# Optimization experiments

Hardware: AMD Instinct MI355X
Metric: run time of the kernel (lower is better)

The kernel has to match this reference:

```python
import jax, jax.numpy as jnp
import numpy as np

S = 2          # scale_int = ceil(scale)
K = 3          # kernel size
OUTC = 3       # num_out_ch
NUM_FEAT = 64


def conv3x3(x, w, b):
    y = jax.lax.conv_general_dilated(x, w, (1, 1), ((1, 1), (1, 1)),
                                     dimension_numbers=('NCHW', 'OIHW', 'NCHW'))
    return y + b[None, :, None, None]


def unfold3x3(x):
    # torch F.unfold(x, 3, padding=1): (N, C*9, H*W), order c*9 + ki*3 + kj
    N, C, H, W = x.shape
    xp = jnp.pad(x, ((0, 0), (0, 0), (1, 1), (1, 1)))
    patches = jnp.stack([xp[:, :, i:i + H, j:j + W]
                         for i in range(3) for j in range(3)], axis=2)  # (N,C,9,H,W)
    return patches.reshape(N, C * 9, H * W)


def setup_inputs() -> dict:
    key = jax.random.key(0)
    ks = jax.random.split(key, 12)
    b, t, c, h, w = 2, 4, 16, 64, 64
    H, W = S * h, S * w
    nf4 = 64 // 4  # 16
    d_w = K * K * NUM_FEAT * OUTC  # 1728
    return {
        'x0': jax.random.normal(ks[0], (b, NUM_FEAT, h, w), jnp.float32),
        'feature': jax.random.normal(ks[1], (b, t, c, h, w), jnp.float32),
        'pos_mat': jax.random.uniform(ks[2], (H, W, 3), jnp.float32),
        'mask': jnp.ones((b, OUTC, H, W), dtype=bool),
        'conv1_w': jax.random.normal(ks[3], (nf4, 64, 3, 3), jnp.float32) * 0.05,
        'conv1_b': jnp.zeros((nf4,), jnp.float32),
        'conv2_w': jax.random.normal(ks[4], (nf4, nf4, 3, 3), jnp.float32) * 0.05,
        'conv2_b': jnp.zeros((nf4,), jnp.float32),
        'f2w1_w': jax.random.normal(ks[5], (256, nf4 + 1), jnp.float32) * 0.05,
        'f2w1_b': jnp.zeros((256,), jnp.float32),
        'f2w2_w': jax.random.normal(ks[6], (d_w, 256), jnp.float32) * 0.05,
        'f2w2_b': jnp.zeros((d_w,), jnp.float32),
    }


def reference(x0, feature, pos_mat, mask, conv1_w, conv1_b, conv2_w, conv2_b,
              f2w1_w, f2w1_b, f2w2_w, f2w2_b):
    b, t, c, h, w = feature.shape
    H, W = S * h, S * w
    # with_gradBack=False -> feature.detach()
    feat = jax.lax.stop_gradient(feature).reshape(b, t * c, h, w)
    # repeat_x(..., upsample=True): nearest-neighbour upsample by S
    feat_up = jnp.repeat(jnp.repeat(feat, S, axis=2), S, axis=3)  # (b,64,H,W)
    f = jax.nn.relu(conv3x3(feat_up, conv1_w, conv1_b))
    f = conv3x3(f, conv2_w, conv2_b)                              # (b,16,H,W)
    pos0 = jnp.transpose(pos_mat, (2, 0, 1))[0:1]                 # (1,H,W)
    fm = jnp.concatenate([f, jnp.broadcast_to(pos0[None], (b, 1, H, W))], axis=1)
    fm = fm.reshape(b, -1, H * W).transpose(0, 2, 1)              # (b,HW,17)
    hdn = jax.nn.relu(fm @ f2w1_w.T + f2w1_b)
    weights = hdn @ f2w2_w.T + f2w2_b                             # (b,HW,1728)
    weights = weights.reshape(b, h, S, w, S, K * K * NUM_FEAT, OUTC)
    weights = jnp.transpose(weights, (0, 2, 4, 1, 3, 5, 6))
    weights = weights.reshape(b, S * S, h * w, K * K * NUM_FEAT, OUTC)
    # repeat_x(x0) tiles x0 S^2 times -> all S^2 col copies identical; compute once
    cols = unfold3x3(x0).transpose(0, 2, 1)                       # (b,hw,576)
    out = jnp.einsum('bpk,bspko->bspo', cols, weights)            # (b,S^2,hw,3)
    out = jnp.transpose(out, (0, 1, 3, 2)).reshape(b, S, S, OUTC, h, w)
    out = jnp.transpose(out, (0, 3, 4, 1, 5, 2)).reshape(b, OUTC, H, W)
    # integer scale -> mask all True -> masked_select + view is identity
    return out, weights
```

## Files before the change

kernel.cpp:

```cpp
#include <hip/hip_runtime.h>

#define THREADS 256

#define Bsz 2
#define HWp 16384
#define Ntot (Bsz*HWp)
#define HID 256
#define Mm 1728
#define FMC 17
#define W_OFF 98304

#define F1_OFF  0
#define F1_SZ   (Bsz*16*HWp)
#define FM_OFF  F1_SZ
#define WB2_OFF (FM_OFF + Ntot*FMC)
#define WB1_OFF (WB2_OFF + (Mm*HID)/2)

typedef __attribute__((ext_vector_type(8))) short bf16x8;
typedef __attribute__((ext_vector_type(4))) float f32x4;

static __device__ __forceinline__ short f2bf(float x) {
    unsigned u = __builtin_bit_cast(unsigned, x);
    unsigned r = (u + 0x7fff + ((u >> 16) & 1)) >> 16;
    return (short)r;
}

__global__ __launch_bounds__(THREADS) void k13_conv1_cvt(const float* __restrict__ feat,
                                                         const float* __restrict__ w1,
                                                         const float* __restrict__ b1,
                                                         float* __restrict__ f1,
                                                         const float* __restrict__ w2g,
                                                         short* __restrict__ wB2,
                                                         const float* __restrict__ w1g,
                                                         short* __restrict__ wB1) {
    int tid = threadIdx.x;
    if (blockIdx.x >= 944) {
        for (int idx = tid; idx < 8192; idx += THREADS) {
            int i = idx & 7, l = (idx >> 3) & 63, h = idx >> 9;
            int k = (l >> 4) * 8 + i, hid = h * 16 + (l & 15);
            wB1[idx] = (k < FMC) ? f2bf(w1g[hid * FMC + k]) : (short)0;
        }
        return;
    }
    if (blockIdx.x >= 512) {
        int t4 = ((blockIdx.x - 512) * THREADS + tid) * 4;
        int i = t4 & 7, l = (t4 >> 3) & 63, ct = (t4 >> 9) & 3, s = (t4 >> 11) & 7, mc = t4 >> 14;
        int col = mc * 64 + ct * 16 + (l & 15);
        int k0 = s * 32 + (l >> 4) * 8 + i;
        f32x4 w = *(const f32x4*)(w2g + col * HID + k0);
        short4 o;
        o.x = f2bf(w[0]); o.y = f2bf(w[1]); o.z = f2bf(w[2]); o.w = f2bf(w[3]);
        *(short4*)(wB2 + t4) = o;
        return;
    }
    __shared__ float sW[4 * 64 * 4];
    int b = blockIdx.x;
    int rg = b & 15, oc = (b >> 4) & 15, bb = b >> 8;
    int c = tid & 63, r = rg * 4 + (tid >> 6);

    #pragma unroll
    for (int q = 0; q < 4; ++q) {
        int e = tid * 4 + q;
        int v = e & 1, u = (e >> 1) & 1, ic = (e >> 2) & 63, pp = (e >> 8) & 3;
        int pi = pp >> 1, pj = pp & 1;
        float s = 0.f;
        for (int ki = 0; ki < 3; ++ki) {
            bool okki = pi ? (u ? (ki == 2) : (ki <= 1)) : (u ? (ki >= 1) : (ki == 0));
            if (!okki) continue;
            for (int kj = 0; kj < 3; ++kj) {
                bool okkj = pj ? (v ? (kj == 2) : (kj <= 1)) : (v ? (kj >= 1) : (kj == 0));
                if (okkj) s += w1[((oc * 64 + ic) * 3 + ki) * 3 + kj];
            }
        }
        sW[(pp * 64 + ic) * 4 + u * 2 + v] = s;
    }
    __syncthreads();

    float bias = b1[oc];
    float a00 = bias, a01 = bias, a10 = bias, a11 = bias;

    float mt = (r > 0) ? 1.f : 0.f, mb2 = (r < 63) ? 1.f : 0.f;
    float ml = (c > 0) ? 1.f : 0.f, mr2 = (c < 63) ? 1.f : 0.f;
    int ro0 = (r > 0) ? -64 : 0, ro2 = (r < 63) ? 64 : 0;
    int co0 = (c > 0) ? -1 : 0, co2 = (c < 63) ? 1 : 0;

    const float* fb = feat + bb * 64 * 4096 + r * 64 + c;
    for (int ic = 0; ic < 64; ++ic) {
        const float* p1 = fb + ic * 4096;
        const float* p0 = p1 + ro0;
        const float* p2 = p1 + ro2;
        float v00 = p0[co0] * (mt * ml), v01 = p0[0] * mt, v02 = p0[co2] * (mt * mr2);
        float v10 = p1[co0] * ml,        v11 = p1[0],      v12 = p1[co2] * mr2;
        float v20 = p2[co0] * (mb2 * ml), v21 = p2[0] * mb2, v22 = p2[co2] * (mb2 * mr2);

        f32x4 w0 = *(const f32x4*)(sW + (0 * 64 + ic) * 4);
        f32x4 w1v = *(const f32x4*)(sW + (1 * 64 + ic) * 4);
        f32x4 w2v = *(const f32x4*)(sW + (2 * 64 + ic) * 4);
        f32x4 w3 = *(const f32x4*)(sW + (3 * 64 + ic) * 4);

        a00 = fmaf(w0[0], v00, a00); a00 = fmaf(w0[1], v01, a00);
        a00 = fmaf(w0[2], v10, a00); a00 = fmaf(w0[3], v11, a00);
        a01 = fmaf(w1v[0], v01, a01); a01 = fmaf(w1v[1], v02, a01);
        a01 = fmaf(w1v[2], v11, a01); a01 = fmaf(w1v[3], v12, a01);
        a10 = fmaf(w2v[0], v10, a10); a10 = fmaf(w2v[1], v11, a10);
        a10 = fmaf(w2v[2], v20, a10); a10 = fmaf(w2v[3], v21, a10);
        a11 = fmaf(w3[0], v11, a11); a11 = fmaf(w3[1], v12, a11);
        a11 = fmaf(w3[2], v21, a11); a11 = fmaf(w3[3], v22, a11);
    }

    float* fo = f1 + (bb * 16 + oc) * HWp + (2 * r) * 128 + 2 * c;
    *reinterpret_cast<float2*>(fo)       = make_float2(fmaxf(a00, 0.f), fmaxf(a01, 0.f));
    *reinterpret_cast<float2*>(fo + 128) = make_float2(fmaxf(a10, 0.f), fmaxf(a11, 0.f));
}

__global__ __launch_bounds__(THREADS) void k35_hdn(const float* __restrict__ f1,
                                                   const float* __restrict__ w2,
                                                   const float* __restrict__ b2,
                                                   const float* __restrict__ pos,
                                                   const short* __restrict__ wB1,
                                                   const float* __restrict__ b1g,
                                                   float* __restrict__ dout) {
    __shared__ float sF[16 * 3 * 68];
    __shared__ float sFM[64 * 33];
    int tid = threadIdx.x;
    int n0 = blockIdx.x * 64;
    int bb = n0 >> 14, tt = n0 & 16383, I = tt >> 7, J0 = tt & 127;

    for (int e = tid; e < 16 * 3 * 68; e += THREADS) {
        int jc = e % 68, r2 = e / 68;
        int di = r2 % 3, ic = r2 / 3;
        int y = I + di - 1, x = J0 + jc - 1;
        float v = 0.f;
        if ((unsigned)y < 128u && (unsigned)x < 128u && jc < 66)
            v = f1[(bb * 16 + ic) * HWp + y * 128 + x];
        sF[(ic * 3 + di) * 68 + jc] = v;
    }
    for (int e = tid; e < 64 * 33; e += THREADS) sFM[e] = 0.f;
    __syncthreads();

    {
        int pix = tid & 63, q = tid >> 6;
        float acc[4];
        #pragma unroll
        for (int o = 0; o < 4; ++o) acc[o] = b2[q * 4 + o];
        #pragma unroll 4
        for (int ic = 0; ic < 16; ++ic) {
            float v[9];
            #pragma unroll
            for (int di = 0; di < 3; ++di) {
                const float* row = sF + (ic * 3 + di) * 68 + pix;
                v[di * 3 + 0] = row[0]; v[di * 3 + 1] = row[1]; v[di * 3 + 2] = row[2];
            }
            #pragma unroll
            for (int o = 0; o < 4; ++o) {
                const float* w = w2 + ((q * 4 + o) * 16 + ic) * 9;
                acc[o] = fmaf(v[0], w[0], acc[o]); acc[o] = fmaf(v[1], w[1], acc[o]);
                acc[o] = fmaf(v[2], w[2], acc[o]); acc[o] = fmaf(v[3], w[3], acc[o]);
                acc[o] = fmaf(v[4], w[4], acc[o]); acc[o] = fmaf(v[5], w[5], acc[o]);
                acc[o] = fmaf(v[6], w[6], acc[o]); acc[o] = fmaf(v[7], w[7], acc[o]);
                acc[o] = fmaf(v[8], w[8], acc[o]);
            }
        }
        #pragma unroll
        for (int o = 0; o < 4; ++o) sFM[pix * 33 + q * 4 + o] = acc[o];
        if (q == 0) sFM[pix * 33 + 16] = pos[(I * 128 + J0 + pix) * 3];
    }
    __syncthreads();

    int w = tid >> 6, l = tid & 63, lm = l & 15, lg = l >> 4;
    int row = w * 16 + lm;
    bf16x8 af;
    #pragma unroll
    for (int i = 0; i < 8; ++i) af[i] = f2bf(sFM[row * 33 + lg * 8 + i]);

    int s0 = (I & 1) * 2, i0 = I >> 1, jmin = J0 >> 1;
    short* sp = (short*)(dout + (size_t)W_OFF +
                         ((size_t)(bb * 4 + s0) * 4096 + i0 * 64 + jmin) * Mm);
    const short* wb = wB1 + l * 8;
    int pbase = ((lg >> 1) * 64 + row) * 8 + (lg & 1) * 4;
    #pragma unroll 4
    for (int h = 0; h < 16; ++h) {
        bf16x8 bfr = *(const bf16x8*)(wb + h * 512);
        f32x4 bias = *(const f32x4*)(b1g + h * 16 + lg * 4);
        f32x4 acc = __builtin_amdgcn_mfma_f32_16x16x32_bf16(bfr, af, bias, 0, 0, 0);
        unsigned c0 = (unsigned short)f2bf(fmaxf(acc[0], 0.f));
        unsigned c1 = (unsigned short)f2bf(fmaxf(acc[1], 0.f));
        unsigned c2 = (unsigned short)f2bf(fmaxf(acc[2], 0.f));
        unsigned c3 = (unsigned short)f2bf(fmaxf(acc[3], 0.f));
        uint2 uv; uv.x = c0 | (c1 << 16); uv.y = c2 | (c3 << 16);
        *(uint2*)(sp + pbase + h * 1024) = uv;
    }
}

__global__ __launch_bounds__(THREADS, 2) void k4_gemm(const short* __restrict__ wB2,
                                                      const float* __restrict__ b2g,
                                                      const float* __restrict__ x0g,
                                                      float* __restrict__ dout) {
    __shared__ short sA[16384];
    __shared__ int   sOB[64];
    __shared__ float sXT[6632];
    __shared__ float sOut[4 * 64 * 3];

    int tid = threadIdx.x;
    int n0 = blockIdx.x * 64;
    int bb = n0 >> 14, tt = n0 & 16383, I = tt >> 7, J0 = tt & 127;
    int s0 = (I & 1) * 2, i0 = I >> 1, jmin = J0 >> 1;

    {
        const short* spc = (const short*)(dout + (size_t)W_OFF +
                             ((size_t)(bb * 4 + s0) * 4096 + i0 * 64 + jmin) * Mm);
        #pragma unroll
        for (int q = 0; q < 8; ++q) {
            int si = (q * 256 + tid) * 8;
            *(bf16x8*)(sA + si) = *(const bf16x8*)(spc + si);
        }
    }
    if (tid < 64) {
        int J = J0 + tid;
        int s = ((I & 1) << 1) | (J & 1);
        int p = ((I >> 1) << 6) | (J >> 1);
        sOB[tid] = W_OFF + ((bb * 4 + s) * 4096 + p) * Mm;
    }
    {
        const float* x0b = x0g + bb * 64 * 4096;
        for (int e = tid; e < 6528; e += THREADS) {
            int ch = e / 102, r2 = e - ch * 102;
            int ki = r2 / 34, jc = r2 - ki * 34;
            int y = i0 + ki - 1, x = jmin + jc - 1;
            float v = 0.f;
            if ((unsigned)y < 64u && (unsigned)x < 64u) v = x0b[(ch * 64 + y) * 64 + x];
            sXT[jc * 195 + ch * 3 + ki] = v;
        }
    }
    __syncthreads();

    int wid = tid >> 6, l = tid & 63;
    int lm = l & 15, lg = l >> 4;
    int lg3 = lg % 3, lg4 = lg * 4;

    int pixbase[4], jl195[4];
    #pragma unroll
    for (int rt = 0; rt < 4; ++rt) {
        pixbase[rt] = sOB[rt * 16 + lm];
        jl195[rt] = (rt * 8 + (lm >> 1)) * 195;
    }

    const short* aptr = sA + lg * 512 + lm * 8;

    float racc[4][3];
    #pragma unroll
    for (int rt = 0; rt < 4; ++rt) {
        racc[rt][0] = 0.f; racc[rt][1] = 0.f; racc[rt][2] = 0.f;
    }

    for (int mc = wid; mc < 27; mc += 4) {
        int m0 = mc * 64;
        f32x4 acc[4][4];
        #pragma unroll
        for (int ct = 0; ct < 4; ++ct) {
            f32x4 bias4 = *(const f32x4*)(b2g + m0 + ct * 16 + lg * 4);
            #pragma unroll
            for (int rt = 0; rt < 4; ++rt)
                acc[rt][ct] = bias4;
        }
        const short* bbase = wB2 + (size_t)mc * 16384 + l * 8;
        #pragma unroll 2
        for (int s = 0; s < 8; ++s) {
            bf16x8 af[4], bfr[4];
            #pragma unroll
            for (int rt = 0; rt < 4; ++rt)
                af[rt] = *(const bf16x8*)(aptr + s * 2048 + rt * 128);
            #pragma unroll
            for (int ct = 0; ct < 4; ++ct)
                bfr[ct] = *(const bf16x8*)(bbase + (s * 4 + ct) * 512);
            #pragma unroll
            for (int rt = 0; rt < 4; ++rt)
                #pragma unroll
                for (int ct = 0; ct < 4; ++ct)
                    acc[rt][ct] = __builtin_amdgcn_mfma_f32_16x16x32_bf16(
                        bfr[ct], af[rt], acc[rt][ct], 0, 0, 0);
        }
        #pragma unroll
        for (int rt = 0; rt < 4; ++rt)
            #pragma unroll
            for (int ct = 0; ct < 4; ++ct)
                *(f32x4*)(dout + pixbase[rt] + m0 + ct * 16 + lg * 4) = acc[rt][ct];
#define ACCUM(QB)                                                              \
        _Pragma("unroll")                                                      \
        for (int ct = 0; ct < 4; ++ct) {                                       \
            int t = m0 + ct * 16 + lg4;                                        \
            int K0 = (t * 21846) >> 16;                                        \
            int rem3 = t - 3 * K0;                                             \
            int Q2 = (K0 * 21846) >> 16;                                       \
            int kja = K0 - 3 * Q2;                                             \
            int kqa = kja * 195 + Q2;                                          \
            int kqb = (kja == 2) ? (Q2 + 1) : (kqa + 195);                     \
            _Pragma("unroll")                                                  \
            for (int rt = 0; rt < 4; ++rt) {                                   \
                float xa = sXT[jl195[rt] + kqa];                               \
                float xb = sXT[jl195[rt] + kqb];                               \
                float x1 = (rem3 == 2) ? xb : xa;                              \
                float x2 = (rem3 >= 1) ? xb : xa;                              \
                racc[rt][(QB + ct) % 3] =                                      \
                    fmaf(acc[rt][ct][0], xa, racc[rt][(QB + ct) % 3]);         \
                racc[rt][(QB + ct + 1) % 3] =                                  \
                    fmaf(acc[rt][ct][1], x1, racc[rt][(QB + ct + 1) % 3]);     \
                racc[rt][(QB + ct + 2) % 3] =                                  \
                    fmaf(acc[rt][ct][2], x2, racc[rt][(QB + ct + 2) % 3]);     \
                racc[rt][(QB + ct) % 3] =                                      \
                    fmaf(acc[rt][ct][3], xb, racc[rt][(QB + ct) % 3]);         \
            }                                                                  \
        }
        switch (mc % 3) {
            case 0: ACCUM(0); break;
            case 1: ACCUM(1); break;
            default: ACCUM(2); break;
        }
#undef ACCUM
    }

    #pragma unroll
    for (int rt = 0; rt < 4; ++rt) {
        float q0 = racc[rt][0], q1 = racc[rt][1], q2 = racc[rt][2];
        float a0 = (lg3 == 0) ? q0 : ((lg3 == 1) ? q2 : q1);
        float a1 = (lg3 == 0) ? q1 : ((lg3 == 1) ? q0 : q2);
        float a2 = (lg3 == 0) ? q2 : ((lg3 == 1) ? q1 : q0);
        a0 += __shfl_xor(a0, 16, 64); a0 += __shfl_xor(a0, 32, 64);
        a1 += __shfl_xor(a1, 16, 64); a1 += __shfl_xor(a1, 32, 64);
        a2 += __shfl_xor(a2, 16, 64); a2 += __shfl_xor(a2, 32, 64);
        if (l < 16) {
            float* so = sOut + (wid * 64 + rt * 16 + lm) * 3;
            so[0] = a0; so[1] = a1; so[2] = a2;
        }
    }
    __syncthreads();
    if (tid < 192) {
        float s = sOut[tid] + sOut[192 + tid] + sOut[384 + tid] + sOut[576 + tid];
        int pix = tid / 3, o = tid - 3 * pix;
        dout[bb * 3 * HWp + o * HWp + I * 128 + J0 + pix] = s;
    }
}

extern "C" void kernel_launch(void* const* d_in, const int* in_sizes, int n_in,
                              void* d_out, int out_size, void* d_ws, size_t ws_size,
                              hipStream_t stream) {
    const float* x0      = (const float*)d_in[0];
    const float* feature = (const float*)d_in[1];
    const float* pos     = (const float*)d_in[2];
    const float* w1      = (const float*)d_in[4];
    const float* b1      = (const float*)d_in[5];
    const float* w2      = (const float*)d_in[6];
    const float* b2      = (const float*)d_in[7];
    const float* f2w1_w  = (const float*)d_in[8];
    const float* f2w1_b  = (const float*)d_in[9];
    const float* f2w2_w  = (const float*)d_in[10];
    const float* f2w2_b  = (const float*)d_in[11];

    float* out = (float*)d_out;
    float* ws  = (float*)d_ws;
    float* f1  = ws + F1_OFF;
    short* wB2 = (short*)(ws + WB2_OFF);
    short* wB1 = (short*)(ws + WB1_OFF);

    k13_conv1_cvt<<<945, THREADS, 0, stream>>>(feature, w1, b1, f1, f2w2_w, wB2,
                                               f2w1_w, wB1);
    k35_hdn<<<Ntot / 64, THREADS, 0, stream>>>(f1, w2, b2, pos, wB1, f2w1_b, out);
    k4_gemm<<<Ntot / 64, THREADS, 0, stream>>>(wB2, f2w2_b, x0, out);
}
```

Measured before the change: 112.5 us.

## Fuse conv2/hidden-layer kernel into the weight GEMM kernel via shared memory

Merges the conv2 + first MLP layer kernel into the second GEMM kernel. The hidden activations are now written straight into the shared-memory A tile, so they no longer make a round trip through global memory. Shared-memory buffers are aliased, and the conv2 input and x0 patch tiles are stored as bf16 to shrink LDS so three blocks can fit per CU. In exchange, the conv2 inputs and unfold values lose precision, and one kernel launch is removed.

```diff
diff --git a/kernel.cpp b/kernel.cpp
--- a/kernel.cpp
+++ b/kernel.cpp
@@ -12,8 +12,7 @@
 
 #define F1_OFF  0
 #define F1_SZ   (Bsz*16*HWp)
-#define FM_OFF  F1_SZ
-#define WB2_OFF (FM_OFF + Ntot*FMC)
+#define WB2_OFF (F1_SZ + Ntot*FMC)
 #define WB1_OFF (WB2_OFF + (Mm*HID)/2)
 
 typedef __attribute__((ext_vector_type(8))) short bf16x8;
@@ -23,6 +22,10 @@
     unsigned u = __builtin_bit_cast(unsigned, x);
     unsigned r = (u + 0x7fff + ((u >> 16) & 1)) >> 16;
     return (short)r;
+}
+static __device__ __forceinline__ float bf2f(short s) {
+    unsigned u = ((unsigned)(unsigned short)s) << 16;
+    return __builtin_bit_cast(float, u);
 }
 
 __global__ __launch_bounds__(THREADS) void k13_conv1_cvt(const float* __restrict__ feat,
@@ -113,29 +116,46 @@
     *reinterpret_cast<float2*>(fo + 128) = make_float2(fmaxf(a10, 0.f), fmaxf(a11, 0.f));
 }
 
-__global__ __launch_bounds__(THREADS) void k35_hdn(const float* __restrict__ f1,
-                                                   const float* __restrict__ w2,
-                                                   const float* __restrict__ b2,
-                                                   const float* __restrict__ pos,
-                                                   const short* __restrict__ wB1,
-                                                   const float* __restrict__ b1g,
-                                                   float* __restrict__ dout) {
-    __shared__ float sF[16 * 3 * 68];
-    __shared__ float sFM[64 * 33];
+__global__ __launch_bounds__(THREADS, 3) void k4_fused(const float* __restrict__ f1,
+                                                       const float* __restrict__ w2,
+                                                       const float* __restrict__ b2,
+                                                       const float* __restrict__ pos,
+                                                       const short* __restrict__ wB1,
+                                                       const float* __restrict__ b1g,
+                                                       const short* __restrict__ wB2,
+                                                       const float* __restrict__ b2g,
+                                                       const float* __restrict__ x0g,
+                                                       float* __restrict__ dout) {
+    __shared__ short sA[16384];
+    __shared__ int   sOB[64];
+    __shared__ float uni[4084];
+
+    short* sF  = (short*)uni;
+    float* sFM = uni + 1584;
+    short* sXT = (short*)uni;
+    float* sOut = uni + 3316;
+
     int tid = threadIdx.x;
     int n0 = blockIdx.x * 64;
     int bb = n0 >> 14, tt = n0 & 16383, I = tt >> 7, J0 = tt & 127;
-
-    for (int e = tid; e < 16 * 3 * 68; e += THREADS) {
-        int jc = e % 68, r2 = e / 68;
+    int i0 = I >> 1, jmin = J0 >> 1;
+
+    for (int e = tid; e < 3168; e += THREADS) {
+        int jc = e % 66, r2 = e / 66;
         int di = r2 % 3, ic = r2 / 3;
         int y = I + di - 1, x = J0 + jc - 1;
         float v = 0.f;
-        if ((unsigned)y < 128u && (unsigned)x < 128u && jc < 66)
+        if ((unsigned)y < 128u && (unsigned)x < 128u)
             v = f1[(bb * 16 + ic) * HWp + y * 128 + x];
-        sF[(ic * 3 + di) * 68 + jc] = v;
-    }
-    for (int e = tid; e < 64 * 33; e += THREADS) sFM[e] = 0.f;
+        sF[(ic * 3 + di) * 66 + jc] = f2bf(v);
+    }
+    for (int e = tid; e < 2112; e += THREADS) sFM[e] = 0.f;
+    if (tid < 64) {
+        int J = J0 + tid;
+        int s = ((I & 1) << 1) | (J & 1);
+        int p = ((I >> 1) << 6) | (J >> 1);
+        sOB[tid] = W_OFF + ((bb * 4 + s) * 4096 + p) * Mm;
+    }
     __syncthreads();
 
     {
@@ -148,8 +168,10 @@
             float v[9];
             #pragma unroll
             for (int di = 0; di < 3; ++di) {
-                const float* row = sF + (ic * 3 + di) * 68 + pix;
-                v[di * 3 + 0] = row[0]; v[di * 3 + 1] = row[1]; v[di * 3 + 2] = row[2];
+                const short* row = sF + (ic * 3 + di) * 66 + pix;
+                v[di * 3 + 0] = bf2f(row[0]);
+                v[di * 3 + 1] = bf2f(row[1]);
+                v[di * 3 + 2] = bf2f(row[2]);
             }
             #pragma unroll
             for (int o = 0; o < 4; ++o) {
@@ -167,59 +189,29 @@
     }
     __syncthreads();
 
-    int w = tid >> 6, l = tid & 63, lm = l & 15, lg = l >> 4;
-    int row = w * 16 + lm;
-    bf16x8 af;
-    #pragma unroll
-    for (int i = 0; i < 8; ++i) af[i] = f2bf(sFM[row * 33 + lg * 8 + i]);
-
-    int s0 = (I & 1) * 2, i0 = I >> 1, jmin = J0 >> 1;
-    short* sp = (short*)(dout + (size_t)W_OFF +
-                         ((size_t)(bb * 4 + s0) * 4096 + i0 * 64 + jmin) * Mm);
-    const short* wb = wB1 + l * 8;
-    int pbase = ((lg >> 1) * 64 + row) * 8 + (lg & 1) * 4;
-    #pragma unroll 4
-    for (int h = 0; h < 16; ++h) {
-        bf16x8 bfr = *(const bf16x8*)(wb + h * 512);
-        f32x4 bias = *(const f32x4*)(b1g + h * 16 + lg * 4);
-        f32x4 acc = __builtin_amdgcn_mfma_f32_16x16x32_bf16(bfr, af, bias, 0, 0, 0);
-        unsigned c0 = (unsigned short)f2bf(fmaxf(acc[0], 0.f));
-        unsigned c1 = (unsigned short)f2bf(fmaxf(acc[1], 0.f));
-        unsigned c2 = (unsigned short)f2bf(fmaxf(acc[2], 0.f));
-        unsigned c3 = (unsigned short)f2bf(fmaxf(acc[3], 0.f));
-        uint2 uv; uv.x = c0 | (c1 << 16); uv.y = c2 | (c3 << 16);
-        *(uint2*)(sp + pbase + h * 1024) = uv;
-    }
-}
-
-__global__ __launch_bounds__(THREADS, 2) void k4_gemm(const short* __restrict__ wB2,
-                                                      const float* __restrict__ b2g,
-                                                      const float* __restrict__ x0g,
-                                                      float* __restrict__ dout) {
-    __shared__ short sA[16384];
-    __shared__ int   sOB[64];
-    __shared__ float sXT[6632];
-    __shared__ float sOut[4 * 64 * 3];
-
-    int tid = threadIdx.x;
-    int n0 = blockIdx.x * 64;
-    int bb = n0 >> 14, tt = n0 & 16383, I = tt >> 7, J0 = tt & 127;
-    int s0 = (I & 1) * 2, i0 = I >> 1, jmin = J0 >> 1;
+    int wv = tid >> 6, l = tid & 63, lm = l & 15, lg = l >> 4;
+
+    int row = wv * 16 + lm;
+    bf16x8 af1;
+    #pragma unroll
+    for (int i = 0; i < 8; ++i) af1[i] = f2bf(sFM[row * 33 + lg * 8 + i]);
+    __syncthreads();
 
     {
-        const short* spc = (const short*)(dout + (size_t)W_OFF +
-                             ((size_t)(bb * 4 + s0) * 4096 + i0 * 64 + jmin) * Mm);
-        #pragma unroll
-        for (int q = 0; q < 8; ++q) {
-            int si = (q * 256 + tid) * 8;
-            *(bf16x8*)(sA + si) = *(const bf16x8*)(spc + si);
-        }
-    }
-    if (tid < 64) {
-        int J = J0 + tid;
-        int s = ((I & 1) << 1) | (J & 1);
-        int p = ((I >> 1) << 6) | (J >> 1);
-        sOB[tid] = W_OFF + ((bb * 4 + s) * 4096 + p) * Mm;
+        const short* wb = wB1 + l * 8;
+        int pbase = ((lg >> 1) * 64 + row) * 8 + (lg & 1) * 4;
+        #pragma unroll 4
+        for (int h = 0; h < 16; ++h) {
+            bf16x8 bfr = *(const bf16x8*)(wb + h * 512);
+            f32x4 bias = *(const f32x4*)(b1g + h * 16 + lg * 4);
+            f32x4 acc = __builtin_amdgcn_mfma_f32_16x16x32_bf16(bfr, af1, bias, 0, 0, 0);
+            unsigned c0 = (unsigned short)f2bf(fmaxf(acc[0], 0.f));
+            unsigned c1 = (unsigned short)f2bf(fmaxf(acc[1], 0.f));
+            unsigned c2 = (unsigned short)f2bf(fmaxf(acc[2], 0.f));
+            unsigned c3 = (unsigned short)f2bf(fmaxf(acc[3], 0.f));
+            uint2 uv; uv.x = c0 | (c1 << 16); uv.y = c2 | (c3 << 16);
+            *(uint2*)(sA + pbase + h * 1024) = uv;
+        }
     }
     {
         const float* x0b = x0g + bb * 64 * 4096;
@@ -229,15 +221,12 @@
             int y = i0 + ki - 1, x = jmin + jc - 1;
             float v = 0.f;
             if ((unsigned)y < 64u && (unsigned)x < 64u) v = x0b[(ch * 64 + y) * 64 + x];
-            sXT[jc * 195 + ch * 3 + ki] = v;
-        }
-    }
-    __syncthreads();
-
-    int wid = tid >> 6, l = tid & 63;
-    int lm = l & 15, lg = l >> 4;
+            sXT[jc * 195 + ch * 3 + ki] = f2bf(v);
+        }
+    }
+    __syncthreads();
+
     int lg3 = lg % 3, lg4 = lg * 4;
-
     int pixbase[4], jl195[4];
     #pragma unroll
     for (int rt = 0; rt < 4; ++rt) {
@@ -253,7 +242,7 @@
         racc[rt][0] = 0.f; racc[rt][1] = 0.f; racc[rt][2] = 0.f;
     }
 
-    for (int mc = wid; mc < 27; mc += 4) {
+    for (int mc = wv; mc < 27; mc += 4) {
         int m0 = mc * 64;
         f32x4 acc[4][4];
         #pragma unroll
@@ -297,8 +286,8 @@
             int kqb = (kja == 2) ? (Q2 + 1) : (kqa + 195);                     \
             _Pragma("unroll")                                                  \
             for (int rt = 0; rt < 4; ++rt) {                                   \
-                float xa = sXT[jl195[rt] + kqa];                               \
-                float xb = sXT[jl195[rt] + kqb];                               \
+                float xa = bf2f(sXT[jl195[rt] + kqa]);                         \
+                float xb = bf2f(sXT[jl195[rt] + kqb]);                         \
                 float x1 = (rem3 == 2) ? xb : xa;                              \
                 float x2 = (rem3 >= 1) ? xb : xa;                              \
                 racc[rt][(QB + ct) % 3] =                                      \
@@ -329,7 +318,7 @@
         a1 += __shfl_xor(a1, 16, 64); a1 += __shfl_xor(a1, 32, 64);
         a2 += __shfl_xor(a2, 16, 64); a2 += __shfl_xor(a2, 32, 64);
         if (l < 16) {
-            float* so = sOut + (wid * 64 + rt * 16 + lm) * 3;
+            float* so = sOut + (wv * 64 + rt * 16 + lm) * 3;
             so[0] = a0; so[1] = a1; so[2] = a2;
         }
     }
@@ -364,6 +353,6 @@
 
     k13_conv1_cvt<<<945, THREADS, 0, stream>>>(feature, w1, b1, f1, f2w2_w, wB2,
                                                f2w1_w, wB1);
-    k35_hdn<<<Ntot / 64, THREADS, 0, stream>>>(f1, w2, b2, pos, wB1, f2w1_b, out);
-    k4_gemm<<<Ntot / 64, THREADS, 0, stream>>>(wB2, f2w2_b, x0, out);
-}
+    k4_fused<<<Ntot / 64, THREADS, 0, stream>>>(f1, w2, b2, pos, wB1, f2w1_b,
+                                                wB2, f2w2_b, x0, out);
+}
```

Result: faster. 108.5 us (-3.5%).
